# Kernel tuning notes

Hardware: AMD Instinct MI355X
Metric: run time of the kernel (lower is better)

## Reference

```python
import jax, jax.numpy as jnp
import numpy as np


def setup_inputs() -> dict:
    key = jax.random.key(0)
    k1, k2, k3, k4 = jax.random.split(key, 4)
    B, N, D, K, O = 8, 6144, 16, 3, 64
    inputs = jax.random.normal(k1, (B, N, D), dtype=jnp.float32)
    supports = jax.random.uniform(k2, (K, N, N), dtype=jnp.float32)
    W = jax.random.normal(k3, (O, D * K), dtype=jnp.float32) * 0.05
    b = jax.random.normal(k4, (O,), dtype=jnp.float32) * 0.05
    return {"inputs": inputs, "supports": supports, "W": W, "b": b}


def reference(inputs, supports, W, b):
    # inputs: [B, N, D]; supports: [K, N, N]; W: [O, D*K]; b: [O]
    B, N, D = inputs.shape
    K = supports.shape[0]
    # matrix_normalization: support + I  (identity self-loop add)
    sup = supports + jnp.eye(N, dtype=supports.dtype)  # [K, N, N]
    # per-support dense matmul; layout [B, N, D, K] matches the torch
    # stack/reshape/transpose chain (feature index = d*K + k)
    y = jnp.einsum('knm,bmd->bndk', sup, inputs)  # [B, N, D, K]
    y = y.reshape(B, N, D * K)
    return y @ W.T + b  # [B, N, O]
```

## Files before the change

### kernel.cpp

```cpp
#include <hip/hip_runtime.h>

#define NN 6144
#define BB 8
#define DD 16
#define KK 3
#define OO 64
#define CCOL 128
#define BND (NN*DD)

typedef short short8 __attribute__((ext_vector_type(8)));
typedef float f32x4 __attribute__((ext_vector_type(4)));

__device__ __forceinline__ short f2bf(float f) {
    unsigned u = __builtin_bit_cast(unsigned, f);
    u = (u + 0x7FFFu + ((u >> 16) & 1u)) >> 16;
    return (short)u;
}

__global__ void __launch_bounds__(256) prep_kernel(
    const float* __restrict__ xin, const float* __restrict__ W,
    unsigned short* __restrict__ Xt, float* __restrict__ Wl)
{
    int g = blockIdx.x * 256 + threadIdx.x;
    if (g < CCOL * NN) {
        int c = g / NN;
        int m = g - c * NN;
        int b = c >> 4, d = c & 15;
        float v = xin[(size_t)b * BND + m * DD + d];
        Xt[g] = (unsigned short)f2bf(v);
    } else if (g < CCOL * NN + OO * 48) {
        int i = g - CCOL * NN;
        int o = i / 48, j = i - o * 48;
        int k = j >> 4, d = j & 15;
        Wl[i] = W[o * 48 + d * 3 + k];
    }
}

__global__ void __launch_bounds__(128) gemm_kernel(
    const float* __restrict__ sup, const float* __restrict__ xin,
    const unsigned short* __restrict__ Xt, float* __restrict__ Yws)
{
    __shared__ short lbuf[8192];

    const int tid = threadIdx.x;
    const int w   = tid >> 6;
    const int L   = tid & 63;
    const int q   = L >> 4;
    const int col = L & 15;
    const int n0  = blockIdx.x * 32;
    const int k   = blockIdx.y;

    const float* A    = sup + (size_t)k * NN * NN;
    const int    nrow = n0 + w * 16 + col;
    const float* arow = A + (size_t)nrow * NN;

    f32x4 acc[8];
#pragma unroll
    for (int i = 0; i < 8; ++i) acc[i] = (f32x4)0.0f;

    for (int m0 = 0; m0 < NN; m0 += 64) {
        const float* ap = arow + m0 + q * 8;
        float4 a0 = *(const float4*)(ap);
        float4 a1 = *(const float4*)(ap + 4);
        float4 a2 = *(const float4*)(ap + 32);
        float4 a3 = *(const float4*)(ap + 36);

#pragma unroll
        for (int i = 0; i < 8; ++i) {
            const unsigned short* src = Xt + (size_t)tid * NN + m0 + i * 8;
            short* dst = &lbuf[(i * 128 + tid) * 8];
            __builtin_amdgcn_global_load_lds(
                (const __attribute__((address_space(1))) unsigned int*)src,
                (__attribute__((address_space(3))) unsigned int*)dst, 16, 0, 0);
        }
        __syncthreads();

        short8 af0, af1;
        af0[0]=f2bf(a0.x); af0[1]=f2bf(a0.y); af0[2]=f2bf(a0.z); af0[3]=f2bf(a0.w);
        af0[4]=f2bf(a1.x); af0[5]=f2bf(a1.y); af0[6]=f2bf(a1.z); af0[7]=f2bf(a1.w);
        af1[0]=f2bf(a2.x); af1[1]=f2bf(a2.y); af1[2]=f2bf(a2.z); af1[3]=f2bf(a2.w);
        af1[4]=f2bf(a3.x); af1[5]=f2bf(a3.y); af1[6]=f2bf(a3.z); af1[7]=f2bf(a3.w);

#pragma unroll
        for (int cc = 0; cc < 8; ++cc) {
            short8 bf = *(const short8*)&lbuf[((0 * 4 + q) * 128 + cc * 16 + col) * 8];
            acc[cc] = __builtin_amdgcn_mfma_f32_16x16x32_bf16(af0, bf, acc[cc], 0, 0, 0);
        }
#pragma unroll
        for (int cc = 0; cc < 8; ++cc) {
            short8 bf = *(const short8*)&lbuf[((1 * 4 + q) * 128 + cc * 16 + col) * 8];
            acc[cc] = __builtin_amdgcn_mfma_f32_16x16x32_bf16(af1, bf, acc[cc], 0, 0, 0);
        }
        __syncthreads();
    }

#pragma unroll
    for (int cc = 0; cc < 8; ++cc) {
#pragma unroll
        for (int r = 0; r < 4; ++r) {
            int nr = n0 + w * 16 + q * 4 + r;
            float v = acc[cc][r] + xin[(size_t)cc * BND + nr * DD + col];
            Yws[((size_t)k * NN + nr) * CCOL + cc * 16 + col] = v;
        }
    }
}

__global__ void __launch_bounds__(256) out_kernel(
    const float* __restrict__ Yws, const float* __restrict__ Wl,
    const float* __restrict__ bias, float* __restrict__ out)
{
    const int o   = threadIdx.x & 63;
    const int wid = blockIdx.x * 4 + (threadIdx.x >> 6);

    float wreg[48];
#pragma unroll
    for (int j = 0; j < 12; ++j)
        *(float4*)&wreg[j * 4] = *(const float4*)&Wl[o * 48 + j * 4];
    const float bv = bias[o];

    for (int ii = 0; ii < 24; ++ii) {
        int p = wid * 24 + ii;
        int b = p / NN;
        int n = p - b * NN;
        const float* yp = Yws + (size_t)n * CCOL + b * 16;
        float acc = bv;
#pragma unroll
        for (int k = 0; k < 3; ++k) {
#pragma unroll
            for (int d4 = 0; d4 < 4; ++d4) {
                float4 y = *(const float4*)(yp + k * (NN * CCOL) + d4 * 4);
                int j = k * 16 + d4 * 4;
                acc += y.x * wreg[j] + y.y * wreg[j + 1] + y.z * wreg[j + 2] + y.w * wreg[j + 3];
            }
        }
        out[(size_t)p * OO + o] = acc;
    }
}

extern "C" void kernel_launch(void* const* d_in, const int* in_sizes, int n_in,
                              void* d_out, int out_size, void* d_ws, size_t ws_size,
                              hipStream_t stream) {
    const float* xin  = (const float*)d_in[0];
    const float* sup  = (const float*)d_in[1];
    const float* W    = (const float*)d_in[2];
    const float* bias = (const float*)d_in[3];
    float* out = (float*)d_out;

    char* ws = (char*)d_ws;
    unsigned short* Xt = (unsigned short*)ws;
    float* Wl  = (float*)(ws + 1572864);
    float* Yws = (float*)(ws + 1585152);

    prep_kernel<<<(CCOL * NN + OO * 48 + 255) / 256, 256, 0, stream>>>(xin, W, Xt, Wl);
    dim3 grid(NN / 32, KK);
    gemm_kernel<<<grid, 128, 0, stream>>>(sup, xin, Xt, Yws);
    out_kernel<<<512, 256, 0, stream>>>(Yws, Wl, bias, out);
}
```

Before: 795.0 us.

## Split-K GEMM across waves with LDS reduction, direct global B loads

Measured after the change: 873.2 us. 9.8% more time.

```diff
diff --git a/kernel.cpp b/kernel.cpp
--- a/kernel.cpp
+++ b/kernel.cpp
@@ -1,12 +1,7 @@
 #include <hip/hip_runtime.h>
 
 #define NN 6144
-#define BB 8
-#define DD 16
-#define KK 3
-#define OO 64
-#define CCOL 128
-#define BND (NN*DD)
+#define BND (NN*16)
 
 typedef short short8 __attribute__((ext_vector_type(8)));
 typedef float f32x4 __attribute__((ext_vector_type(4)));
@@ -18,95 +13,86 @@
 }
 
 __global__ void __launch_bounds__(256) prep_kernel(
-    const float* __restrict__ xin, const float* __restrict__ W,
-    unsigned short* __restrict__ Xt, float* __restrict__ Wl)
+    const float* __restrict__ xin, unsigned short* __restrict__ Xt)
 {
-    int g = blockIdx.x * 256 + threadIdx.x;
-    if (g < CCOL * NN) {
-        int c = g / NN;
-        int m = g - c * NN;
-        int b = c >> 4, d = c & 15;
-        float v = xin[(size_t)b * BND + m * DD + d];
-        Xt[g] = (unsigned short)f2bf(v);
-    } else if (g < CCOL * NN + OO * 48) {
-        int i = g - CCOL * NN;
-        int o = i / 48, j = i - o * 48;
-        int k = j >> 4, d = j & 15;
-        Wl[i] = W[o * 48 + d * 3 + k];
+    __shared__ unsigned short ldsT[16 * 64];
+    const int b  = blockIdx.y;
+    const int m0 = blockIdx.x * 64;
+    const int t  = threadIdx.x;
+    const int ml = t >> 2, dq = t & 3;
+    float4 v = *(const float4*)(xin + (size_t)b * BND + (size_t)(m0 + ml) * 16 + dq * 4);
+    ldsT[(dq * 4 + 0) * 64 + ml] = (unsigned short)f2bf(v.x);
+    ldsT[(dq * 4 + 1) * 64 + ml] = (unsigned short)f2bf(v.y);
+    ldsT[(dq * 4 + 2) * 64 + ml] = (unsigned short)f2bf(v.z);
+    ldsT[(dq * 4 + 3) * 64 + ml] = (unsigned short)f2bf(v.w);
+    __syncthreads();
+    if (t < 128) {
+        int d = t >> 3, j = t & 7;
+        short8 s = *(const short8*)&ldsT[d * 64 + j * 8];
+        *(short8*)(Xt + (size_t)(b * 16 + d) * NN + m0 + j * 8) = s;
     }
 }
 
-__global__ void __launch_bounds__(128) gemm_kernel(
+__global__ void __launch_bounds__(256, 4) gemm_kernel(
     const float* __restrict__ sup, const float* __restrict__ xin,
     const unsigned short* __restrict__ Xt, float* __restrict__ Yws)
 {
-    __shared__ short lbuf[8192];
-
+    __shared__ float lred[4 * 2048];
     const int tid = threadIdx.x;
-    const int w   = tid >> 6;
-    const int L   = tid & 63;
-    const int q   = L >> 4;
-    const int col = L & 15;
-    const int n0  = blockIdx.x * 32;
-    const int k   = blockIdx.y;
-
-    const float* A    = sup + (size_t)k * NN * NN;
-    const int    nrow = n0 + w * 16 + col;
-    const float* arow = A + (size_t)nrow * NN;
+    const int w = tid >> 6, L = tid & 63, q = L >> 4, col = L & 15;
+    const int n0 = blockIdx.x * 16;
+    const int k  = blockIdx.y;
+    const float* arow = sup + (size_t)k * NN * NN + (size_t)(n0 + col) * NN;
+    const unsigned short* xcol = Xt + (size_t)col * NN;
 
     f32x4 acc[8];
 #pragma unroll
     for (int i = 0; i < 8; ++i) acc[i] = (f32x4)0.0f;
 
-    for (int m0 = 0; m0 < NN; m0 += 64) {
-        const float* ap = arow + m0 + q * 8;
-        float4 a0 = *(const float4*)(ap);
-        float4 a1 = *(const float4*)(ap + 4);
-        float4 a2 = *(const float4*)(ap + 32);
-        float4 a3 = *(const float4*)(ap + 36);
-
+    int m0 = w * 1536 + q * 8;
+    for (int it = 0; it < 48; ++it, m0 += 32) {
+        float4 a0 = *(const float4*)(arow + m0);
+        float4 a1 = *(const float4*)(arow + m0 + 4);
+        short8 bfr[8];
 #pragma unroll
-        for (int i = 0; i < 8; ++i) {
-            const unsigned short* src = Xt + (size_t)tid * NN + m0 + i * 8;
-            short* dst = &lbuf[(i * 128 + tid) * 8];
-            __builtin_amdgcn_global_load_lds(
-                (const __attribute__((address_space(1))) unsigned int*)src,
-                (__attribute__((address_space(3))) unsigned int*)dst, 16, 0, 0);
-        }
-        __syncthreads();
-
-        short8 af0, af1;
-        af0[0]=f2bf(a0.x); af0[1]=f2bf(a0.y); af0[2]=f2bf(a0.z); af0[3]=f2bf(a0.w);
-        af0[4]=f2bf(a1.x); af0[5]=f2bf(a1.y); af0[6]=f2bf(a1.z); af0[7]=f2bf(a1.w);
-        af1[0]=f2bf(a2.x); af1[1]=f2bf(a2.y); af1[2]=f2bf(a2.z); af1[3]=f2bf(a2.w);
-        af1[4]=f2bf(a3.x); af1[5]=f2bf(a3.y); af1[6]=f2bf(a3.z); af1[7]=f2bf(a3.w);
-
+        for (int cc = 0; cc < 8; ++cc)
+            bfr[cc] = *(const short8*)(xcol + (size_t)cc * 16 * NN + m0);
+        short8 af;
+        af[0] = f2bf(a0.x); af[1] = f2bf(a0.y); af[2] = f2bf(a0.z); af[3] = f2bf(a0.w);
+        af[4] = f2bf(a1.x); af[5] = f2bf(a1.y); af[6] = f2bf(a1.z); af[7] = f2bf(a1.w);
 #pragma unroll
-        for (int cc = 0; cc < 8; ++cc) {
-            short8 bf = *(const short8*)&lbuf[((0 * 4 + q) * 128 + cc * 16 + col) * 8];
-            acc[cc] = __builtin_amdgcn_mfma_f32_16x16x32_bf16(af0, bf, acc[cc], 0, 0, 0);
-        }
-#pragma unroll
-        for (int cc = 0; cc < 8; ++cc) {
-            short8 bf = *(const short8*)&lbuf[((1 * 4 + q) * 128 + cc * 16 + col) * 8];
-            acc[cc] = __builtin_amdgcn_mfma_f32_16x16x32_bf16(af1, bf, acc[cc], 0, 0, 0);
-        }
-        __syncthreads();
+        for (int cc = 0; cc < 8; ++cc)
+            acc[cc] = __builtin_amdgcn_mfma_f32_16x16x32_bf16(af, bfr[cc], acc[cc], 0, 0, 0);
     }
 
 #pragma unroll
-    for (int cc = 0; cc < 8; ++cc) {
+    for (int cc = 0; cc < 8; ++cc)
 #pragma unroll
-        for (int r = 0; r < 4; ++r) {
-            int nr = n0 + w * 16 + q * 4 + r;
-            float v = acc[cc][r] + xin[(size_t)cc * BND + nr * DD + col];
-            Yws[((size_t)k * NN + nr) * CCOL + cc * 16 + col] = v;
-        }
+        for (int r = 0; r < 4; ++r)
+            lred[w * 2048 + (q * 4 + r) * 128 + cc * 16 + col] = acc[cc][r];
+    __syncthreads();
+
+#pragma unroll
+    for (int half = 0; half < 2; ++half) {
+        int e = half * 1024 + tid * 4;
+        float4 s0 = *(const float4*)&lred[e];
+        float4 s1 = *(const float4*)&lred[2048 + e];
+        float4 s2 = *(const float4*)&lred[4096 + e];
+        float4 s3 = *(const float4*)&lred[6144 + e];
+        int r = e >> 7, c = e & 127;
+        int n = n0 + r, b = c >> 4, d = c & 15;
+        float4 xi = *(const float4*)(xin + (size_t)b * BND + (size_t)n * 16 + d);
+        float4 o;
+        o.x = s0.x + s1.x + s2.x + s3.x + xi.x;
+        o.y = s0.y + s1.y + s2.y + s3.y + xi.y;
+        o.z = s0.z + s1.z + s2.z + s3.z + xi.z;
+        o.w = s0.w + s1.w + s2.w + s3.w + xi.w;
+        *(float4*)(Yws + ((size_t)k * NN + n) * 128 + c) = o;
     }
 }
 
 __global__ void __launch_bounds__(256) out_kernel(
-    const float* __restrict__ Yws, const float* __restrict__ Wl,
+    const float* __restrict__ Yws, const float* __restrict__ W,
     const float* __restrict__ bias, float* __restrict__ out)
 {
     const int o   = threadIdx.x & 63;
@@ -114,26 +100,27 @@
 
     float wreg[48];
 #pragma unroll
-    for (int j = 0; j < 12; ++j)
-        *(float4*)&wreg[j * 4] = *(const float4*)&Wl[o * 48 + j * 4];
+    for (int d = 0; d < 16; ++d)
+#pragma unroll
+        for (int kk = 0; kk < 3; ++kk)
+            wreg[kk * 16 + d] = W[o * 48 + d * 3 + kk];
     const float bv = bias[o];
 
     for (int ii = 0; ii < 24; ++ii) {
         int p = wid * 24 + ii;
         int b = p / NN;
         int n = p - b * NN;
-        const float* yp = Yws + (size_t)n * CCOL + b * 16;
+        const float* yp = Yws + (size_t)n * 128 + b * 16;
         float acc = bv;
 #pragma unroll
-        for (int k = 0; k < 3; ++k) {
+        for (int kk = 0; kk < 3; ++kk)
 #pragma unroll
             for (int d4 = 0; d4 < 4; ++d4) {
-                float4 y = *(const float4*)(yp + k * (NN * CCOL) + d4 * 4);
-                int j = k * 16 + d4 * 4;
+                float4 y = *(const float4*)(yp + (size_t)kk * (NN * 128) + d4 * 4);
+                int j = kk * 16 + d4 * 4;
                 acc += y.x * wreg[j] + y.y * wreg[j + 1] + y.z * wreg[j + 2] + y.w * wreg[j + 3];
             }
-        }
-        out[(size_t)p * OO + o] = acc;
+        out[(size_t)p * 64 + o] = acc;
     }
 }
 
@@ -148,11 +135,9 @@
 
     char* ws = (char*)d_ws;
     unsigned short* Xt = (unsigned short*)ws;
-    float* Wl  = (float*)(ws + 1572864);
-    float* Yws = (float*)(ws + 1585152);
+    float* Yws = (float*)(ws + 1572864);
 
-    prep_kernel<<<(CCOL * NN + OO * 48 + 255) / 256, 256, 0, stream>>>(xin, W, Xt, Wl);
-    dim3 grid(NN / 32, KK);
-    gemm_kernel<<<grid, 128, 0, stream>>>(sup, xin, Xt, Yws);
-    out_kernel<<<512, 256, 0, stream>>>(Yws, Wl, bias, out);
+    prep_kernel<<<dim3(96, 8), 256, 0, stream>>>(xin, Xt);
+    gemm_kernel<<<dim3(384, 3), 256, 0, stream>>>(sup, xin, Xt, Yws);
+    out_kernel<<<512, 256, 0, stream>>>(Yws, W, bias, out);
 }
```
